# Performance work log

Measured on AMD Instinct MI355X. Metric: run time of the kernel, lower is better.

Reference implementation:

```python
import jax, jax.numpy as jnp
import numpy as np

BLOCK = 32


def _dct_constants(bs):
    # Replicates get_dct_constants + the sorting/reshaping done in DCTEncoderLayer.__init__
    x, y = np.meshgrid(np.arange(bs), np.arange(bs), indexing='xy')
    basis = np.zeros((bs, bs, bs, bs), dtype=np.float32)
    mag = np.zeros((bs, bs), dtype=np.float64)
    fac = np.zeros((bs, bs), dtype=np.float32)
    for v in range(bs):
        for u in range(bs):
            xb = np.cos((2 * x + 1) * u * np.pi / (2 * bs))
            yb = np.cos((2 * y + 1) * v * np.pi / (2 * bs))
            basis[v, u] = (xb * yb).astype(np.float32)
            mag[v, u] = np.linalg.norm(np.array([v, u], dtype=np.int64))
            c_v = 1 / np.sqrt(2) if v == 0 else 1.0
            c_u = 1 / np.sqrt(2) if u == 0 else 1.0
            fac[v, u] = c_u * c_v
    kernels = basis.reshape(-1, bs, bs)
    factors = fac.reshape(-1)
    idx = np.argsort(mag.reshape(-1))  # same default argsort as the torch module
    return kernels[idx].astype(np.float32), factors[idx].astype(np.float32)


def setup_inputs() -> dict:
    key = jax.random.key(0)
    rgb = jax.random.uniform(key, (32, 3, 512, 512), dtype=jnp.float32)
    kernels, factors = _dct_constants(BLOCK)
    return {
        "rgb_images_batch": rgb,
        "kernels": jnp.asarray(kernels),   # [K=bs^2, bs, bs], sorted by freq magnitude
        "factors": jnp.asarray(factors),   # [K]
    }


def _rgb_to_ycbcr(rgb):
    # kornia.color.rgb_to_ycbcr (delta = 0.5)
    r, g, b = rgb[:, 0], rgb[:, 1], rgb[:, 2]
    y = 0.299 * r + 0.587 * g + 0.114 * b
    cb = (b - y) * 0.564 + 0.5
    cr = (r - y) * 0.713 + 0.5
    return jnp.stack([y, cb, cr], axis=1)  # [B,3,H,W]


def reference(rgb_images_batch, kernels, factors):
    bs = BLOCK
    B, C, H, W = rgb_images_batch.shape
    nh, nw = H // bs, W // bs
    ycbcr = 2.0 * _rgb_to_ycbcr(rgb_images_batch) - 1.0            # [B,3,H,W]
    # non-overlapping blocks: [B,3,nh,nw,bs,bs]
    blocks = ycbcr.reshape(B, 3, nh, bs, nw, bs).transpose(0, 1, 2, 4, 3, 5)
    # stride=bs conv2d with dense DCT basis kernels == per-block contraction
    coeffs = jnp.einsum('bcmnxy,kxy->bckmn', blocks, kernels)      # [B,3,K,nh,nw]
    scale = (2.0 / bs) * factors                                   # [K]
    coeffs = coeffs * scale[None, None, :, None, None]
    # torch.cat([y, cb, cr], dim=1) -> [B, 3*K, nh, nw]
    return coeffs.reshape(B, 3 * bs * bs, nh, nw)
```

## Files before the change

### kernel.cpp

```cpp
#include <hip/hip_runtime.h>
#include <math.h>


typedef __bf16 bf16x8 __attribute__((ext_vector_type(8)));
typedef float  f32x4  __attribute__((ext_vector_type(4)));

#define PI_F 3.14159265358979323846f

__device__ __forceinline__ unsigned short f2bf(float f) {
    union { float f; unsigned u; } v; v.f = f;
    unsigned u = v.u;
    u += 0x7fffu + ((u >> 16) & 1u);
    return (unsigned short)(u >> 16);
}

__global__ __launch_bounds__(256) void setup_kernel(const float* __restrict__ kern,
                                                    const float* __restrict__ factors,
                                                    unsigned short* __restrict__ Cbf,
                                                    int2* __restrict__ T2) {
    int k = blockIdx.x * 256 + threadIdx.x;
    int i = k & 31, t = k >> 5;
    Cbf[k] = f2bf(cosf((float)((2 * i + 1) * t) * (PI_F / 64.f)));

    float k00 = kern[(size_t)k * 1024];
    float rv  = kern[(size_t)k * 1024 + 32] / k00;
    float ru  = kern[(size_t)k * 1024 + 1]  / k00;
    float cv2 = fminf(fmaxf((rv + 3.f) * 0.25f, 0.f), 1.f);
    float cu2 = fminf(fmaxf((ru + 3.f) * 0.25f, 0.f), 1.f);
    int v = __float2int_rn(acosf(sqrtf(cv2)) * (64.f / PI_F));
    int u = __float2int_rn(acosf(sqrtf(cu2)) * (64.f / PI_F));
    float s = factors[k] * (2.f / 32.f);
    T2[v * 32 + u] = make_int2(k, __float_as_int(s));
}

__global__ __launch_bounds__(512, 4) void dct_fused(const float* __restrict__ rgb,
                                                    const unsigned short* __restrict__ Cbf,
                                                    const int2* __restrict__ T2,
                                                    float* __restrict__ out) {
    __shared__ __align__(16) unsigned char Tls[32 * 1280];

    const int tid  = threadIdx.x;
    const int lane = tid & 63;
    const int w    = tid >> 6;
    const int quad = lane >> 4;
    const int l15  = lane & 15;
    const int b    = blockIdx.x >> 4;
    const int loc  = blockIdx.x & 15;
    const int m    = ((loc & 7) << 1) | (loc >> 3);

    union { bf16x8 v; unsigned short s[8]; } af0, af1;
    af0.v = *(const bf16x8*)(Cbf + l15 * 32 + quad * 8);
    af1.v = *(const bf16x8*)(Cbf + (16 + l15) * 32 + quad * 8);

    const f32x4 zero = {0.f, 0.f, 0.f, 0.f};

    bf16x8 fr[3][4];
    const float* rbase = rgb + (size_t)b * 786432 + (size_t)l15 * 32 + (size_t)quad * 8;
#pragma unroll
    for (int xi = 0; xi < 4; ++xi) {
        const int x = w * 4 + xi;
        const float* p = rbase + (size_t)(m * 32 + x) * 512;
        float4 R0 = *(const float4*)(p);
        float4 R1 = *(const float4*)(p + 4);
        float4 G0 = *(const float4*)(p + 262144);
        float4 G1 = *(const float4*)(p + 262148);
        float4 B0 = *(const float4*)(p + 524288);
        float4 B1 = *(const float4*)(p + 524292);
        float R[8]  = {R0.x, R0.y, R0.z, R0.w, R1.x, R1.y, R1.z, R1.w};
        float G[8]  = {G0.x, G0.y, G0.z, G0.w, G1.x, G1.y, G1.z, G1.w};
        float Bv[8] = {B0.x, B0.y, B0.z, B0.w, B1.x, B1.y, B1.z, B1.w};
        union { bf16x8 v; unsigned short s[8]; } fy, fcb, fcr;
#pragma unroll
        for (int e = 0; e < 8; ++e) {
            float y = 0.299f * R[e] + 0.587f * G[e] + 0.114f * Bv[e];
            fy.s[e]  = f2bf(2.f * y - 1.f);
            fcb.s[e] = f2bf(1.128f * (Bv[e] - y));
            fcr.s[e] = f2bf(1.426f * (R[e] - y));
        }
        fr[0][xi] = fy.v;
        fr[1][xi] = fcb.v;
        fr[2][xi] = fcr.v;
    }

    const size_t obase0 = (size_t)(b * 3) * 262144 + (size_t)m * 16 + (size_t)l15;
#pragma unroll
    for (int c = 0; c < 3; ++c) {
#pragma unroll
        for (int fh = 0; fh < 2; ++fh) {
            f32x4 dd[4];
#pragma unroll
            for (int xi = 0; xi < 4; ++xi)
                dd[xi] = __builtin_amdgcn_mfma_f32_16x16x32_bf16(
                    fh ? af1.v : af0.v, fr[c][xi], zero, 0, 0, 0);
#pragma unroll
            for (int r = 0; r < 4; ++r) {
                const int f1 = fh * 16 + quad * 4 + r;
                ushort4 pk;
                pk.x = f2bf(dd[0][r]);
                pk.y = f2bf(dd[1][r]);
                pk.z = f2bf(dd[2][r]);
                pk.w = f2bf(dd[3][r]);
                *(ushort4*)(Tls + f1 * 1280 + l15 * 80 + w * 8) = pk;
            }
        }
        __syncthreads();

        const size_t obase = obase0 + (size_t)c * 262144;
#pragma unroll
        for (int i = 0; i < 4; ++i) {
            const int f1 = w * 4 + i;
            bf16x8 bfr = *(const bf16x8*)(Tls + f1 * 1280 + l15 * 80 + quad * 16);
#pragma unroll
            for (int uh = 0; uh < 2; ++uh) {
                f32x4 d2 = __builtin_amdgcn_mfma_f32_16x16x32_bf16(
                    uh ? af1.v : af0.v, bfr, zero, 0, 0, 0);
                const int f2b = uh * 16 + quad * 4;
#pragma unroll
                for (int r = 0; r < 4; ++r) {
                    int2 ks = T2[(f2b + r) * 32 + f1];
                    out[obase + (size_t)ks.x * 256] = d2[r] * __int_as_float(ks.y);
                }
            }
        }
        __syncthreads();
    }
}

extern "C" void kernel_launch(void* const* d_in, const int* in_sizes, int n_in,
                              void* d_out, int out_size, void* d_ws, size_t ws_size,
                              hipStream_t stream) {
    const float* rgb     = (const float*)d_in[0];
    const float* kern    = (const float*)d_in[1];
    const float* factors = (const float*)d_in[2];
    float* out = (float*)d_out;

    unsigned short* Cbf = (unsigned short*)d_ws;
    int2* T2 = (int2*)((char*)d_ws + 8192);

    setup_kernel<<<4, 256, 0, stream>>>(kern, factors, Cbf, T2);
    dct_fused<<<512, 512, 0, stream>>>(rgb, Cbf, T2, out);
}
```

Before: 217.9 us.

## Split color channels across blocks and vectorize permuted index-table loads

Each block now handles a single YCbCr channel, so the grid triples and the per-block channel loop with its extra barriers is removed. The color conversion is folded into one fused linear combination per channel. The index/scale table is permuted so each lane fetches its eight entries with four 16-byte loads instead of scattered 8-byte loads. The launch bound hint rises to 8 blocks per SM. The cost is that each RGB pixel is now read three times from memory instead of once, which relies on the L2/cache to absorb the extra reads.

```diff
diff --git a/kernel.cpp b/kernel.cpp
--- a/kernel.cpp
+++ b/kernel.cpp
@@ -30,10 +30,11 @@
     int v = __float2int_rn(acosf(sqrtf(cv2)) * (64.f / PI_F));
     int u = __float2int_rn(acosf(sqrtf(cu2)) * (64.f / PI_F));
     float s = factors[k] * (2.f / 32.f);
-    T2[v * 32 + u] = make_int2(k, __float_as_int(s));
+    int vq = (v >> 2) & 3, vh = v >> 4, vr = v & 3;
+    T2[(u * 4 + vq) * 8 + vh * 4 + vr] = make_int2(k, __float_as_int(s));
 }
 
-__global__ __launch_bounds__(512, 4) void dct_fused(const float* __restrict__ rgb,
+__global__ __launch_bounds__(512, 8) void dct_fused(const float* __restrict__ rgb,
                                                     const unsigned short* __restrict__ Cbf,
                                                     const int2* __restrict__ T2,
                                                     float* __restrict__ out) {
@@ -44,8 +45,11 @@
     const int w    = tid >> 6;
     const int quad = lane >> 4;
     const int l15  = lane & 15;
-    const int b    = blockIdx.x >> 4;
-    const int loc  = blockIdx.x & 15;
+    const int g    = blockIdx.x;
+    const int bc   = g >> 4;
+    const int b    = bc / 3;
+    const int c    = bc - b * 3;
+    const int loc  = g & 15;
     const int m    = ((loc & 7) << 1) | (loc >> 3);
 
     union { bf16x8 v; unsigned short s[8]; } af0, af1;
@@ -54,7 +58,12 @@
 
     const f32x4 zero = {0.f, 0.f, 0.f, 0.f};
 
-    bf16x8 fr[3][4];
+    float ar, ag, ab, ao;
+    if (c == 0)      { ar =  0.598f;     ag =  1.174f;     ab =  0.228f;     ao = -1.f; }
+    else if (c == 1) { ar = -0.337272f;  ag = -0.662136f;  ab =  0.999408f;  ao =  0.f; }
+    else             { ar =  0.999626f;  ag = -0.837062f;  ab = -0.162564f;  ao =  0.f; }
+
+    bf16x8 fr[4];
     const float* rbase = rgb + (size_t)b * 786432 + (size_t)l15 * 32 + (size_t)quad * 8;
 #pragma unroll
     for (int xi = 0; xi < 4; ++xi) {
@@ -69,60 +78,53 @@
         float R[8]  = {R0.x, R0.y, R0.z, R0.w, R1.x, R1.y, R1.z, R1.w};
         float G[8]  = {G0.x, G0.y, G0.z, G0.w, G1.x, G1.y, G1.z, G1.w};
         float Bv[8] = {B0.x, B0.y, B0.z, B0.w, B1.x, B1.y, B1.z, B1.w};
-        union { bf16x8 v; unsigned short s[8]; } fy, fcb, fcr;
+        union { bf16x8 v; unsigned short s[8]; } f;
 #pragma unroll
         for (int e = 0; e < 8; ++e) {
-            float y = 0.299f * R[e] + 0.587f * G[e] + 0.114f * Bv[e];
-            fy.s[e]  = f2bf(2.f * y - 1.f);
-            fcb.s[e] = f2bf(1.128f * (Bv[e] - y));
-            fcr.s[e] = f2bf(1.426f * (R[e] - y));
+            float val = ar * R[e] + ag * G[e] + ab * Bv[e] + ao;
+            f.s[e] = f2bf(val);
         }
-        fr[0][xi] = fy.v;
-        fr[1][xi] = fcb.v;
-        fr[2][xi] = fcr.v;
+        fr[xi] = f.v;
     }
 
-    const size_t obase0 = (size_t)(b * 3) * 262144 + (size_t)m * 16 + (size_t)l15;
 #pragma unroll
-    for (int c = 0; c < 3; ++c) {
+    for (int fh = 0; fh < 2; ++fh) {
+        f32x4 dd[4];
 #pragma unroll
-        for (int fh = 0; fh < 2; ++fh) {
-            f32x4 dd[4];
+        for (int xi = 0; xi < 4; ++xi)
+            dd[xi] = __builtin_amdgcn_mfma_f32_16x16x32_bf16(
+                fh ? af1.v : af0.v, fr[xi], zero, 0, 0, 0);
 #pragma unroll
-            for (int xi = 0; xi < 4; ++xi)
-                dd[xi] = __builtin_amdgcn_mfma_f32_16x16x32_bf16(
-                    fh ? af1.v : af0.v, fr[c][xi], zero, 0, 0, 0);
+        for (int r = 0; r < 4; ++r) {
+            const int f1 = fh * 16 + quad * 4 + r;
+            ushort4 pk;
+            pk.x = f2bf(dd[0][r]);
+            pk.y = f2bf(dd[1][r]);
+            pk.z = f2bf(dd[2][r]);
+            pk.w = f2bf(dd[3][r]);
+            *(ushort4*)(Tls + f1 * 1280 + l15 * 80 + w * 8) = pk;
+        }
+    }
+    __syncthreads();
+
+    const size_t obase = (size_t)bc * 262144 + (size_t)m * 16 + (size_t)l15;
+#pragma unroll
+    for (int i = 0; i < 4; ++i) {
+        const int f1 = w * 4 + i;
+        union { int4 q[4]; int2 e[8]; } tt;
+        const int4* tp = (const int4*)(T2 + ((f1 * 4 + quad) << 3));
+        tt.q[0] = tp[0]; tt.q[1] = tp[1]; tt.q[2] = tp[2]; tt.q[3] = tp[3];
+        bf16x8 bfr = *(const bf16x8*)(Tls + f1 * 1280 + l15 * 80 + quad * 16);
+#pragma unroll
+        for (int uh = 0; uh < 2; ++uh) {
+            f32x4 d2 = __builtin_amdgcn_mfma_f32_16x16x32_bf16(
+                uh ? af1.v : af0.v, bfr, zero, 0, 0, 0);
 #pragma unroll
             for (int r = 0; r < 4; ++r) {
-                const int f1 = fh * 16 + quad * 4 + r;
-                ushort4 pk;
-                pk.x = f2bf(dd[0][r]);
-                pk.y = f2bf(dd[1][r]);
-                pk.z = f2bf(dd[2][r]);
-                pk.w = f2bf(dd[3][r]);
-                *(ushort4*)(Tls + f1 * 1280 + l15 * 80 + w * 8) = pk;
+                int2 ks = tt.e[uh * 4 + r];
+                out[obase + (size_t)ks.x * 256] = d2[r] * __int_as_float(ks.y);
             }
         }
-        __syncthreads();
-
-        const size_t obase = obase0 + (size_t)c * 262144;
-#pragma unroll
-        for (int i = 0; i < 4; ++i) {
-            const int f1 = w * 4 + i;
-            bf16x8 bfr = *(const bf16x8*)(Tls + f1 * 1280 + l15 * 80 + quad * 16);
-#pragma unroll
-            for (int uh = 0; uh < 2; ++uh) {
-                f32x4 d2 = __builtin_amdgcn_mfma_f32_16x16x32_bf16(
-                    uh ? af1.v : af0.v, bfr, zero, 0, 0, 0);
-                const int f2b = uh * 16 + quad * 4;
-#pragma unroll
-                for (int r = 0; r < 4; ++r) {
-                    int2 ks = T2[(f2b + r) * 32 + f1];
-                    out[obase + (size_t)ks.x * 256] = d2[r] * __int_as_float(ks.y);
-                }
-            }
-        }
-        __syncthreads();
     }
 }
 
@@ -138,5 +140,5 @@
     int2* T2 = (int2*)((char*)d_ws + 8192);
 
     setup_kernel<<<4, 256, 0, stream>>>(kern, factors, Cbf, T2);
-    dct_fused<<<512, 512, 0, stream>>>(rgb, Cbf, T2, out);
+    dct_fused<<<1536, 512, 0, stream>>>(rgb, Cbf, T2, out);
 }
```

Result: no change. 213.8 us (-1.9%).
